# Performance work log

Hardware: AMD Instinct MI355X
Metric: run time of the kernel (lower is better)

Reference implementation:

```python
import jax, jax.numpy as jnp
import numpy as np

B, S, V, L, H, NH, NL = 4, 256, 64, 10, 128, 8, 3
DH = H // NH
LP1 = L + 1


def setup_inputs() -> dict:
    key = jax.random.key(0)
    ks = jax.random.split(key, 18)
    sc = 1.0 / np.sqrt(H)
    return {
        "x": jax.random.normal(ks[0], (B, S, V), jnp.float32),
        "adjacency_logits": jax.random.normal(ks[1], (V, V, LP1), jnp.float32) * 0.1,
        "var_emb": jax.random.normal(ks[2], (V, H), jnp.float32),
        "temp_emb": jax.random.normal(ks[3], (LP1, H), jnp.float32),
        "mech_W": jax.random.normal(ks[4], (V, NL, H, H), jnp.float32) * sc,
        "mech_b": jax.random.normal(ks[5], (V, NL, H), jnp.float32) * 0.01,
        "ln_g": jnp.ones((V, NL, H), jnp.float32),
        "ln_b": jnp.zeros((V, NL, H), jnp.float32),
        "Wq": jax.random.normal(ks[6], (V, H, H), jnp.float32) * sc,
        "Wk": jax.random.normal(ks[7], (V, H, H), jnp.float32) * sc,
        "Wv": jax.random.normal(ks[8], (V, H, H), jnp.float32) * sc,
        "Wo": jax.random.normal(ks[9], (V, H, H), jnp.float32) * sc,
        "bq": jnp.zeros((V, H), jnp.float32),
        "bk": jnp.zeros((V, H), jnp.float32),
        "bv": jnp.zeros((V, H), jnp.float32),
        "bo": jnp.zeros((V, H), jnp.float32),
        "out_W": jax.random.normal(ks[10], (V, H), jnp.float32) * sc,
        "out_b": jnp.zeros((V,), jnp.float32),
    }


def reference(x, adjacency_logits, var_emb, temp_emb, mech_W, mech_b, ln_g, ln_b,
              Wq, Wk, Wv, Wo, bq, bk, bv, bo, out_W, out_b):
    b, s, v = x.shape
    lp1 = adjacency_logits.shape[-1]
    adj = jax.nn.sigmoid(adjacency_logits)  # (V_src, V_tgt, L+1), soft adjacency

    # xlag[b,t,src,l] = x[b, t-l, src] with zero padding (the shift-pad loop, fused)
    xlag = jnp.stack([jnp.pad(x, ((0, 0), (l, 0), (0, 0)))[:, :s] for l in range(lp1)], axis=-1)

    # causal_input[b,t,tgt,h] = sum_{src,l} xlag * adj[src,tgt,l] * (var_emb[src,h] + temp_emb[l,h])
    A = jnp.einsum('btsl,sil->btis', xlag, adj)   # contracted over lag
    Bl = jnp.einsum('btsl,sil->btil', xlag, adj)  # contracted over source
    z = jnp.einsum('btis,sh->btih', A, var_emb) + jnp.einsum('btil,lh->btih', Bl, temp_emb)  # (B,S,V,H)

    # per-variable causal mechanism: Linear -> LayerNorm -> GELU (dropout = identity at eval)
    eps = 1e-5
    nl = mech_W.shape[1]
    for li in range(nl):
        z = jnp.einsum('btvh,vhk->btvk', z, mech_W[:, li]) + mech_b[:, li]
        mu = z.mean(axis=-1, keepdims=True)
        var = z.var(axis=-1, keepdims=True)
        z = (z - mu) / jnp.sqrt(var + eps) * ln_g[:, li] + ln_b[:, li]
        z = jax.nn.gelu(z, approximate=False)

    # per-variable multi-head self-attention over the sequence axis
    def heads(t):
        return t.reshape(b, s, v, NH, DH)
    q = heads(jnp.einsum('btvh,vhk->btvk', z, Wq) + bq)
    k = heads(jnp.einsum('btvh,vhk->btvk', z, Wk) + bk)
    vv = heads(jnp.einsum('btvh,vhk->btvk', z, Wv) + bv)
    scores = jnp.einsum('bqvnd,bkvnd->bvnqk', q, k) / np.sqrt(DH)  # (B,V,NH,S,S)
    attn = jax.nn.softmax(scores, axis=-1)
    o = jnp.einsum('bvnqk,bkvnd->bqvnd', attn, vv).reshape(b, s, v, NH * DH)
    o = jnp.einsum('btvh,vhk->btvk', o, Wo) + bo

    # per-variable output head Linear(H, 1), concatenated over variables
    predictions = jnp.einsum('btvh,vh->btv', o, out_W) + out_b  # (B,S,V)
    return predictions
```

## Files before the change

### kernel.cpp

```cpp
#include <hip/hip_runtime.h>
#include <math.h>

#define BB   4
#define SS   256
#define VV   64
#define LP1  11
#define HH   128
#define NHH  8
#define DHH  16
#define NLL  3
#define BSZ  1024

typedef unsigned short u16;
typedef unsigned int   u32;
typedef __attribute__((ext_vector_type(8))) short s16x8;
typedef __attribute__((ext_vector_type(4))) float f32x4;

__device__ __forceinline__ float bfbits2f(u32 hi16) {
    u32 i = hi16 << 16; float f; __builtin_memcpy(&f, &i, 4); return f;
}
__device__ __forceinline__ u16 f2bf(float f) {
    u32 i; __builtin_memcpy(&i, &f, 4);
    return (u16)((i + 0x7fffu + ((i >> 16) & 1u)) >> 16);
}
__device__ __forceinline__ u16 f2bf_trunc(float f) {
    u32 i; __builtin_memcpy(&i, &f, 4);
    return (u16)(i >> 16);
}
__device__ __forceinline__ u32 cvtpk(float lo, float hi) {
    u32 r;
    asm("v_cvt_pk_bf16_f32 %0, %1, %2" : "=v"(r) : "v"(lo), "v"(hi));
    return r;
}
__device__ __forceinline__ float ldf(const void* p, size_t i, int isbf) {
    if (isbf) return bfbits2f(((const u16*)p)[i]);
    return ((const float*)p)[i];
}
__device__ __forceinline__ float4 ld4(const void* p, size_t i, int isbf) {
    float4 v;
    if (isbf) {
        uint2 u = *(const uint2*)((const u16*)p + i);
        v.x = bfbits2f(u.x & 0xffffu); v.y = bfbits2f(u.x >> 16);
        v.z = bfbits2f(u.y & 0xffffu); v.w = bfbits2f(u.y >> 16);
    } else {
        v = *(const float4*)((const float*)p + i);
    }
    return v;
}
__device__ __forceinline__ void gll16(const u16* g, u16* l) {
    __builtin_amdgcn_global_load_lds(
        (const __attribute__((address_space(1))) void*)g,
        (__attribute__((address_space(3))) void*)l, 16, 0, 0);
}

__global__ __launch_bounds__(64) void k_sniff(const u16* __restrict__ probe,
                                              int* __restrict__ flags) {
    if (threadIdx.x == 0) {
        int wild = 0;
        for (int j = 0; j < 256; j++) {
            float v = bfbits2f(probe[j]);
            if (!(fabsf(v) < 1e8f)) wild = 1;
        }
        flags[0] = wild ? 0 : 1;
    }
}

__global__ __launch_bounds__(256) void k_adj(const void* __restrict__ logits,
                                             float* __restrict__ adj,
                                             const int* __restrict__ flags) {
    int isbf = flags[0];
    int i = blockIdx.x * 256 + threadIdx.x;
    if (i < VV * VV * LP1) {
        float v = ldf(logits, i, isbf);
        adj[i] = 1.f / (1.f + expf(-v));
    }
}

__global__ __launch_bounds__(128) void k_fuse(const void* __restrict__ Wo,
                                              const void* __restrict__ outW,
                                              const void* __restrict__ bo,
                                              const void* __restrict__ outb,
                                              float* __restrict__ wfused,
                                              float* __restrict__ bfused,
                                              const int* __restrict__ flags) {
    int isbf = flags[0];
    int v = blockIdx.x; int h = threadIdx.x;
    __shared__ float ow[HH];
    __shared__ float red[HH];
    ow[h] = ldf(outW, (size_t)v * HH + h, isbf);
    __syncthreads();
    size_t wb = ((size_t)v * HH + h) * HH;
    float acc = 0.f;
    #pragma unroll 8
    for (int k = 0; k < HH; k++) acc += ldf(Wo, wb + k, isbf) * ow[k];
    wfused[v * HH + h] = acc;
    red[h] = ldf(bo, (size_t)v * HH + h, isbf) * ow[h];
    __syncthreads();
    for (int s = 64; s > 0; s >>= 1) { if (h < s) red[h] += red[h + s]; __syncthreads(); }
    if (h == 0) bfused[v] = red[0] + ldf(outb, v, isbf);
}

struct WPack {
    const void* src[6];
    u16* dh[6];
    u16* dl[6];
};
#define TP 136
__global__ __launch_bounds__(256) void k_wprep(WPack wp,
                                               const int* __restrict__ flags) {
    int isbf = flags[0];
    int mat = blockIdx.x;
    int tid = threadIdx.x;
    if (mat >= 384) {
        if (mat == 384) {
            const void* raw = wp.src[4];
            u16* dh = wp.dh[4]; u16* dl = wp.dl[4];
            int n = tid >> 1, half = tid & 1;
            for (int i = 0; i < 32; i++) {
                int s = half * 32 + i;
                float val = ldf(raw, (size_t)s * HH + n, isbf);
                u16 hi = f2bf(val);
                int dst = n * 64 + (s ^ ((n & 7) * 8));
                dh[dst] = hi;
                dl[dst] = f2bf(val - bfbits2f(hi));
            }
        } else {
            const void* raw = wp.src[5];
            u16* dh = wp.dh[5]; u16* dl = wp.dl[5];
            for (int p = tid; p < 8192; p += 256) { dh[p] = 0; dl[p] = 0; }
            __syncthreads();
            if (tid < HH) {
                int n = tid;
                for (int l = 0; l < LP1; l++) {
                    float val = ldf(raw, (size_t)l * HH + n, isbf);
                    u16 hi = f2bf(val);
                    int dst = n * 64 + (l ^ ((n & 7) * 8));
                    dh[dst] = hi;
                    dl[dst] = f2bf(val - bfbits2f(hi));
                }
            }
        }
        return;
    }
    int seg = (mat < 192) ? 0 : 1 + ((mat - 192) >> 6);
    int rel = (mat < 192) ? mat : ((mat - 192) & 63);
    const void* raw = wp.src[seg];
    u16* Wh = wp.dh[seg];
    u16* Wl = wp.dl[seg];
    size_t src = (size_t)rel * (HH * HH);
    if (isbf) {
        __shared__ u16 tile[HH * TP];
        const uint4* sp = (const uint4*)((const u16*)raw + src);
        #pragma unroll
        for (int u = 0; u < 8; u++) {
            int p = u * 256 + tid;
            int h = p >> 4, k8 = (p & 15) * 8;
            int k8s = k8 ^ ((((u32)h >> 3) & 15) * 8);
            *(uint4*)&tile[h * TP + k8s] = sp[p];
        }
        __syncthreads();
        #pragma unroll
        for (int u = 0; u < 8; u++) {
            int p = u * 256 + tid;
            int kcol = p >> 4, h8 = (p & 15) * 8;
            u16 vals[8];
            #pragma unroll
            for (int j = 0; j < 8; j++) {
                int h = h8 + j;
                int ks = kcol ^ ((((u32)h >> 3) & 15) * 8);
                vals[j] = tile[h * TP + ks];
            }
            uint4 pk;
            pk.x = (u32)vals[0] | ((u32)vals[1] << 16);
            pk.y = (u32)vals[2] | ((u32)vals[3] << 16);
            pk.z = (u32)vals[4] | ((u32)vals[5] << 16);
            pk.w = (u32)vals[6] | ((u32)vals[7] << 16);
            int c = h8 >> 6;
            int kloc = (h8 & 63) ^ ((kcol & 7) * 8);
            *(uint4*)&Wh[src + c * 8192 + kcol * 64 + kloc] = pk;
        }
    } else {
        int kcol = tid >> 1, h0 = (tid & 1) * 64;
        for (int i = 0; i < 64; i++) {
            int h = h0 + i;
            float w = ldf(raw, src + (size_t)h * HH + kcol, 0);
            u16 hi = f2bf(w);
            int c = h >> 6;
            size_t dst = src + c * 8192 + (size_t)kcol * 64 + ((h & 63) ^ ((kcol & 7) * 8));
            Wh[dst] = hi;
            Wl[dst] = f2bf(w - bfbits2f(hi));
        }
    }
}

#define PB  72
__global__ __launch_bounds__(256) void k_mega(
    const void* __restrict__ x, const float* __restrict__ adjp,
    const u16* __restrict__ VeH, const u16* __restrict__ VeL,
    const u16* __restrict__ TeH, const u16* __restrict__ TeL,
    const u16* __restrict__ WmH, const u16* __restrict__ WmL,
    const u16* __restrict__ WqH, const u16* __restrict__ WqL,
    const u16* __restrict__ WkH, const u16* __restrict__ WkL,
    const u16* __restrict__ WvH, const u16* __restrict__ WvL,
    const void* __restrict__ mechb,
    const void* __restrict__ lng, const void* __restrict__ lnb,
    const void* __restrict__ bq, const void* __restrict__ bk,
    const void* __restrict__ bv,
    u16* __restrict__ Qh, u16* __restrict__ Ql,
    u16* __restrict__ Ko, u16* __restrict__ Vt,
    const int* __restrict__ flags)
{
    __shared__ __align__(16) u16 SMEM[32768];
    u16* Az_h = SMEM;
    u16* Az_l = SMEM + 8192;
    u16* BdS  = SMEM + 16384;
    u16* Vt_sh = BdS;

    int isbf = flags[0];
    int wexact = isbf;
    int tid = threadIdx.x;
    int bid = blockIdx.x;
    int xcd = bid & 7, idx = bid >> 3;
    int v = xcd * 8 + (idx >> 4);
    int tile = idx & 15;
    int b = tile >> 2, t0 = (tile & 3) * 64;
    int wave = tid >> 6, lane = tid & 63;
    int quad = lane >> 4, l15 = lane & 15;
    int m0 = wave * 16;
    int swzl = (l15 & 7) * 8;

    float* xt = (float*)SMEM;
    for (int p = tid; p < 74 * 64; p += 256) {
        int rr = p >> 6, s = p & 63;
        int trow = t0 - 10 + rr;
        float val = (trow >= 0) ? ldf(x, (size_t)(b * SS + trow) * VV + s, isbf) : 0.f;
        xt[s * 81 + rr] = val;
    }
    __syncthreads();

    float* A_f = (float*)BdS;
    float* Blp = A_f + 64 * 68;
    float* Blf = Blp + 64 * 44;
    {
        int t = lane;
        int sg = wave;
        float blp[LP1];
        #pragma unroll
        for (int l = 0; l < LP1; l++) blp[l] = 0.f;
        for (int k = 0; k < 16; k++) {
            int s = sg * 16 + k;
            const float* ap = adjp + (s * VV + v) * LP1;
            float xw[LP1];
            #pragma unroll
            for (int j = 0; j < LP1; j++) xw[j] = xt[s * 81 + t + j];
            float a = 0.f;
            #pragma unroll
            for (int l = 0; l < LP1; l++) {
                float pr = xw[10 - l] * ap[l];
                a += pr; blp[l] += pr;
            }
            A_f[t * 68 + s] = a;
        }
        #pragma unroll
        for (int l = 0; l < LP1; l++) Blp[t * 44 + sg * 11 + l] = blp[l];
    }
    __syncthreads();
    {
        int t = tid >> 2, c0 = (tid & 3) * 4;
        #pragma unroll
        for (int c = c0; c < c0 + 4; c++) {
            float s4 = 0.f;
            if (c < LP1)
                s4 = (Blp[t * 44 + c] + Blp[t * 44 + 11 + c]) +
                     (Blp[t * 44 + 22 + c] + Blp[t * 44 + 33 + c]);
            Blf[t * 16 + c] = s4;
        }
    }
    __syncthreads();

    s16x8 ahf[2], alf[2], blh, bll;
    #pragma unroll
    for (int kk = 0; kk < 2; kk++) {
        #pragma unroll
        for (int j = 0; j < 8; j++) {
            float a = A_f[(m0 + l15) * 68 + kk * 32 + quad * 8 + j];
            u32 w = cvtpk(a, a);
            u16 hi = (u16)(w & 0xffffu);
            ahf[kk][j] = (short)hi;
            float res = a - bfbits2f(hi);
            alf[kk][j] = (short)(cvtpk(res, res) & 0xffffu);
        }
    }
    #pragma unroll
    for (int j = 0; j < 8; j++) {
        float a = (quad < 2) ? Blf[(m0 + l15) * 16 + quad * 8 + j] : 0.f;
        u32 w = cvtpk(a, a);
        u16 hi = (u16)(w & 0xffffu);
        blh[j] = (short)hi;
        float res = a - bfbits2f(hi);
        bll[j] = (short)(cvtpk(res, res) & 0xffffu);
    }
    __syncthreads();

    auto stageB = [&](u16* dst, const u16* g) {
        const u16* gl = g + wave * 2048 + lane * 8;
        u16* lb = dst + wave * 2048;
        #pragma unroll
        for (int u = 0; u < 4; u++)
            gll16(gl + u * 512, lb + u * 512);
    };

    f32x4 acc[8];
    #pragma unroll
    for (int nt = 0; nt < 8; nt++) {
        f32x4 zz = {0.f, 0.f, 0.f, 0.f};
        acc[nt] = zz;
    }

    if (wexact) {
        stageB(BdS, VeH);
        stageB(BdS + 8192, TeH);
        __syncthreads();
        #pragma unroll
        for (int kk = 0; kk < 2; kk++) {
            int bcol = (kk * 32 + quad * 8) ^ swzl;
            #pragma unroll
            for (int nt = 0; nt < 8; nt++) {
                s16x8 bh = *(const s16x8*)&BdS[(nt * 16 + l15) * 64 + bcol];
                acc[nt] = __builtin_amdgcn_mfma_f32_16x16x32_bf16(ahf[kk], bh, acc[nt], 0, 0, 0);
                acc[nt] = __builtin_amdgcn_mfma_f32_16x16x32_bf16(alf[kk], bh, acc[nt], 0, 0, 0);
            }
        }
        {
            int bcol = (quad * 8) ^ swzl;
            #pragma unroll
            for (int nt = 0; nt < 8; nt++) {
                s16x8 th = *(const s16x8*)&BdS[8192 + (nt * 16 + l15) * 64 + bcol];
                acc[nt] = __builtin_amdgcn_mfma_f32_16x16x32_bf16(blh, th, acc[nt], 0, 0, 0);
                acc[nt] = __builtin_amdgcn_mfma_f32_16x16x32_bf16(bll, th, acc[nt], 0, 0, 0);
            }
        }
    } else {
        stageB(BdS, VeH);
        stageB(BdS + 8192, VeL);
        __syncthreads();
        #pragma unroll
        for (int kk = 0; kk < 2; kk++) {
            int bcol = (kk * 32 + quad * 8) ^ swzl;
            #pragma unroll
            for (int nt = 0; nt < 8; nt++) {
                s16x8 bh = *(const s16x8*)&BdS[(nt * 16 + l15) * 64 + bcol];
                s16x8 bl = *(const s16x8*)&BdS[8192 + (nt * 16 + l15) * 64 + bcol];
                acc[nt] = __builtin_amdgcn_mfma_f32_16x16x32_bf16(ahf[kk], bh, acc[nt], 0, 0, 0);
                acc[nt] = __builtin_amdgcn_mfma_f32_16x16x32_bf16(alf[kk], bh, acc[nt], 0, 0, 0);
                acc[nt] = __builtin_amdgcn_mfma_f32_16x16x32_bf16(ahf[kk], bl, acc[nt], 0, 0, 0);
            }
        }
        __syncthreads();
        stageB(BdS, TeH);
        stageB(BdS + 8192, TeL);
        __syncthreads();
        {
            int bcol = (quad * 8) ^ swzl;
            #pragma unroll
            for (int nt = 0; nt < 8; nt++) {
                s16x8 th = *(const s16x8*)&BdS[(nt * 16 + l15) * 64 + bcol];
                s16x8 tl = *(const s16x8*)&BdS[8192 + (nt * 16 + l15) * 64 + bcol];
                acc[nt] = __builtin_amdgcn_mfma_f32_16x16x32_bf16(blh, th, acc[nt], 0, 0, 0);
                acc[nt] = __builtin_amdgcn_mfma_f32_16x16x32_bf16(bll, th, acc[nt], 0, 0, 0);
                acc[nt] = __builtin_amdgcn_mfma_f32_16x16x32_bf16(blh, tl, acc[nt], 0, 0, 0);
            }
        }
    }
    __syncthreads();

    #pragma unroll
    for (int r = 0; r < 4; r++) {
        int rloc = m0 + quad * 4 + r;
        int swr = (rloc & 7) * 8;
        #pragma unroll
        for (int nt = 0; nt < 8; nt++) {
            float val = acc[nt][r];
            float sx = __shfl_xor(val, 1);
            u32 w = cvtpk(val, sx);
            float res = val - bfbits2f(w & 0xffffu);
            float rx = __shfl_xor(res, 1);
            u32 wl = cvtpk(res, rx);
            if (!(l15 & 1)) {
                int colw = (nt * 16 + (l15 & ~1)) ^ swr;
                *(u32*)&Az_h[rloc * 128 + colw] = w;
                *(u32*)&Az_l[rloc * 128 + colw] = wl;
            }
        }
    }

    int shift = wexact ? 1 : 2;
    int PER = 1 << shift;
    int NCH = 6 << shift;

    auto wchunk = [&](int ch) -> const u16* {
        int li = ch >> shift;
        int sub = ch & (PER - 1);
        int cc = sub & 1, lo = sub >> 1;
        const u16* p; size_t wb;
        if (li < 3)       { p = lo ? WmL : WmH; wb = (size_t)(v * NLL + li) * 16384; }
        else if (li == 3) { p = lo ? WqL : WqH; wb = (size_t)v * 16384; }
        else if (li == 4) { p = lo ? WkL : WkH; wb = (size_t)v * 16384; }
        else              { p = lo ? WvL : WvH; wb = (size_t)v * 16384; }
        return p + wb + cc * 8192;
    };

    auto epilogue = [&](int li) {
        float bcol[8], gcol[8], b2col[8];
        #pragma unroll
        for (int nt = 0; nt < 8; nt++) {
            int col = nt * 16 + l15;
            if (li < 3) {
                size_t pb = (size_t)v * (NLL * HH) + (size_t)li * HH + col;
                bcol[nt]  = ldf(mechb, pb, isbf);
                gcol[nt]  = ldf(lng, pb, isbf);
                b2col[nt] = ldf(lnb, pb, isbf);
            } else {
                const void* bp = (li == 3) ? bq : (li == 4) ? bk : bv;
                bcol[nt] = ldf(bp, (size_t)v * HH + col, isbf);
            }
        }
        if (li == 5) __syncthreads();
        #pragma unroll
        for (int r = 0; r < 4; r++) {
            float vals[8];
            float sum = 0.f, sq = 0.f;
            #pragma unroll
            for (int nt = 0; nt < 8; nt++) {
                float val = acc[nt][r] + bcol[nt];
                vals[nt] = val; sum += val; sq += val * val;
            }
            int rloc = m0 + quad * 4 + r;
            if (li < 3) {
                #pragma unroll
                for (int m = 1; m < 16; m <<= 1) {
                    sum += __shfl_xor(sum, m);
                    sq  += __shfl_xor(sq, m);
                }
                float mean = sum * (1.f / HH);
                float var  = sq * (1.f / HH) - mean * mean;
                float rstd = rsqrtf(var + 1e-5f);
                int swr = (rloc & 7) * 8;
                #pragma unroll
                for (int nt = 0; nt < 8; nt++) {
                    float y = (vals[nt] - mean) * rstd * gcol[nt] + b2col[nt];
                    y = 0.5f * y * (1.f + erff(y * 0.70710678118654752f));
                    float sx = __shfl_xor(y, 1);
                    u32 w = cvtpk(y, sx);
                    float res = y - bfbits2f(w & 0xffffu);
                    float rx = __shfl_xor(res, 1);
                    u32 wl = cvtpk(res, rx);
                    if (!(l15 & 1)) {
                        int colw = (nt * 16 + (l15 & ~1)) ^ swr;
                        *(u32*)&Az_h[rloc * 128 + colw] = w;
                        *(u32*)&Az_l[rloc * 128 + colw] = wl;
                    }
                }
            } else if (li == 3) {
                int row = tile * 64 + rloc;
                size_t ob = ((size_t)v * BSZ + row) * HH;
                #pragma unroll
                for (int nt = 0; nt < 8; nt++) {
                    float val = vals[nt];
                    float sx = __shfl_xor(val, 1);
                    u32 w = cvtpk(val, sx);
                    float res = val - bfbits2f(w & 0xffffu);
                    float rx = __shfl_xor(res, 1);
                    u32 wl = cvtpk(res, rx);
                    if (!(l15 & 1)) {
                        size_t oi = ob + nt * 16 + (l15 & ~1);
                        *(u32*)&Qh[oi] = w;
                        *(u32*)&Ql[oi] = wl;
                    }
                }
            } else if (li == 4) {
                int row = tile * 64 + rloc;
                size_t ob = ((size_t)v * BSZ + row) * HH;
                #pragma unroll
                for (int nt = 0; nt < 8; nt++) {
                    u32 h = f2bf(vals[nt]);
                    u32 hx = (u32)__shfl_xor((int)h, 1);
                    if (!(l15 & 1))
                        *(u32*)&Ko[ob + nt * 16 + (l15 & ~1)] = h | (hx << 16);
                }
            } else {
                #pragma unroll
                for (int nt = 0; nt < 8; nt++)
                    Vt_sh[(nt * 16 + l15) * PB + rloc] = f2bf(vals[nt]);
            }
        }
        if (li == 5) {
            __syncthreads();
            int col = tid >> 1, half = tid & 1;
            int n = col >> 4, d = col & 15;
            int bb = tile >> 2, tq = (tile & 3) * 64;
            size_t dst = (((size_t)(v * BB + bb) * NHH + n) * DHH + d) * SS + tq + half * 32;
            #pragma unroll
            for (int j = 0; j < 4; j++)
                *(uint4*)&Vt[dst + j * 8] = *(const uint4*)&Vt_sh[col * PB + half * 32 + j * 8];
        }
    };

    stageB(BdS, wchunk(0));
    __syncthreads();

    for (int ch = 0; ch < NCH; ch++) {
        int bsel = ch & 1;
        if (ch + 1 < NCH) stageB(BdS + (bsel ^ 1) * 8192, wchunk(ch + 1));
        int sub = ch & (PER - 1);
        int li = ch >> shift;
        int cc = sub & 1, lo = sub >> 1;
        if (sub == 0) {
            #pragma unroll
            for (int nt = 0; nt < 8; nt++) {
                f32x4 zz = {0.f, 0.f, 0.f, 0.f};
                acc[nt] = zz;
            }
        }
        const u16* Bp = BdS + bsel * 8192;
        #pragma unroll
        for (int kk = 0; kk < 2; kk++) {
            int acol = (cc * 64 + kk * 32 + quad * 8) ^ swzl;
            int bcol = (kk * 32 + quad * 8) ^ swzl;
            s16x8 ah = *(const s16x8*)&Az_h[(m0 + l15) * 128 + acol];
            if (!lo) {
                s16x8 al = *(const s16x8*)&Az_l[(m0 + l15) * 128 + acol];
                #pragma unroll
                for (int nt = 0; nt < 8; nt++) {
                    s16x8 bh = *(const s16x8*)&Bp[(nt * 16 + l15) * 64 + bcol];
                    acc[nt] = __builtin_amdgcn_mfma_f32_16x16x32_bf16(ah, bh, acc[nt], 0, 0, 0);
                    acc[nt] = __builtin_amdgcn_mfma_f32_16x16x32_bf16(al, bh, acc[nt], 0, 0, 0);
                }
            } else {
                #pragma unroll
                for (int nt = 0; nt < 8; nt++) {
                    s16x8 bl = *(const s16x8*)&Bp[(nt * 16 + l15) * 64 + bcol];
                    acc[nt] = __builtin_amdgcn_mfma_f32_16x16x32_bf16(ah, bl, acc[nt], 0, 0, 0);
                }
            }
        }
        if (sub == PER - 1) epilogue(li);
        __syncthreads();
    }
}

#define LDW 40
__global__ __launch_bounds__(256) void k_attn2(const u16* __restrict__ Qh,
                                               const u16* __restrict__ Ql,
                                               const u16* __restrict__ K16,
                                               const u16* __restrict__ Vt,
                                               float* __restrict__ O) {
    __shared__ u16 Kp_sh[SS * LDW];
    __shared__ u16 Vt_sh[DHH * 264];
    __shared__ u16 P_sh[4][16 * LDW];
    int tid = threadIdx.x;
    int wave = tid >> 6, lane = tid & 63;
    int quad = lane >> 4, l15 = lane & 15;
    int bn = blockIdx.x, v = blockIdx.y;
    int b = bn >> 3, n = bn & 7;
    size_t qkbase = ((size_t)v * BSZ + b * SS) * HH + n * DHH;
    size_t vtbase = ((size_t)(v * BB + b) * NHH + n) * DHH * SS;

    {
        int row = tid;
        uint4 k0 = *(const uint4*)&K16[qkbase + (size_t)row * HH];
        uint4 k1 = *(const uint4*)&K16[qkbase + (size_t)row * HH + 8];
        *(uint4*)&Kp_sh[row * LDW + 0]  = k0;
        *(uint4*)&Kp_sh[row * LDW + 8]  = k1;
        *(uint4*)&Kp_sh[row * LDW + 16] = k0;
        *(uint4*)&Kp_sh[row * LDW + 24] = k1;
    }
    #pragma unroll
    for (int u = 0; u < 2; u++) {
        int p = u * 256 + tid;
        int d = p >> 5, su = (p & 31) * 8;
        *(uint4*)&Vt_sh[d * 264 + su] = *(const uint4*)&Vt[vtbase + (size_t)d * SS + su];
    }
    __syncthreads();

    s16x8 ones;
    #pragma unroll
    for (int i = 0; i < 8; i++) ones[i] = (short)0x3F80;

    for (int mt = wave * 4; mt < wave * 4 + 4; mt++) {
        const u16* Qsrc = (quad < 2) ? Qh : Ql;
        s16x8 aq = *(const s16x8*)&Qsrc[qkbase + (size_t)(mt * 16 + l15) * HH + (quad & 1) * 8];
        f32x4 oacc = {0.f, 0.f, 0.f, 0.f};
        f32x4 lacc = {0.f, 0.f, 0.f, 0.f};
        for (int jt2 = 0; jt2 < 8; jt2++) {
            #pragma unroll
            for (int sub = 0; sub < 2; sub++) {
                int jt = jt2 * 2 + sub;
                s16x8 bk = *(const s16x8*)&Kp_sh[(jt * 16 + l15) * LDW + quad * 8];
                f32x4 s = {0.f, 0.f, 0.f, 0.f};
                s = __builtin_amdgcn_mfma_f32_16x16x32_bf16(aq, bk, s, 0, 0, 0);
                #pragma unroll
                for (int r = 0; r < 4; r++) {
                    float p = __expf(s[r] * 0.25f);
                    P_sh[wave][(quad * 4 + r) * LDW + sub * 16 + l15] = f2bf_trunc(p);
                }
            }
            s16x8 ap = *(const s16x8*)&P_sh[wave][l15 * LDW + quad * 8];
            s16x8 bv = *(const s16x8*)&Vt_sh[l15 * 264 + jt2 * 32 + quad * 8];
            oacc = __builtin_amdgcn_mfma_f32_16x16x32_bf16(ap, bv, oacc, 0, 0, 0);
            lacc = __builtin_amdgcn_mfma_f32_16x16x32_bf16(ap, ones, lacc, 0, 0, 0);
        }
        #pragma unroll
        for (int r = 0; r < 4; r++) {
            float val = oacc[r] / lacc[r];
            O[((size_t)v * BSZ + b * SS + mt * 16 + quad * 4 + r) * HH + n * DHH + l15] = val;
        }
    }
}

__global__ __launch_bounds__(256) void k_final(const float* __restrict__ o,
                                               const float* __restrict__ wfused,
                                               const float* __restrict__ bfused,
                                               void* __restrict__ out,
                                               const int* __restrict__ flags) {
    __shared__ float wf[HH];
    int isbf = flags[0];
    int tid = threadIdx.x; int b = blockIdx.x; int v = blockIdx.y;
    if (tid < HH) wf[tid] = wfused[v * HH + tid];
    __syncthreads();
    int rg = tid >> 3;
    int l8 = tid & 7;
    float4 w0 = *(const float4*)&wf[l8 * 16];
    float4 w1 = *(const float4*)&wf[l8 * 16 + 4];
    float4 w2 = *(const float4*)&wf[l8 * 16 + 8];
    float4 w3 = *(const float4*)&wf[l8 * 16 + 12];
    float bv = bfused[v];
    #pragma unroll
    for (int pass = 0; pass < 8; pass++) {
        int bt = b * SS + pass * 32 + rg;
        const float4* orow = (const float4*)(o + ((size_t)v * BSZ + bt) * HH + l8 * 16);
        float4 a0 = orow[0], a1 = orow[1], a2 = orow[2], a3 = orow[3];
        float acc = a0.x * w0.x + a0.y * w0.y + a0.z * w0.z + a0.w * w0.w
                  + a1.x * w1.x + a1.y * w1.y + a1.z * w1.z + a1.w * w1.w
                  + a2.x * w2.x + a2.y * w2.y + a2.z * w2.z + a2.w * w2.w
                  + a3.x * w3.x + a3.y * w3.y + a3.z * w3.z + a3.w * w3.w;
        acc += __shfl_xor(acc, 1);
        acc += __shfl_xor(acc, 2);
        acc += __shfl_xor(acc, 4);
        if (l8 == 0) {
            float pred = acc + bv;
            size_t oi = (size_t)bt * VV + v;
            if (isbf) ((u16*)out)[oi] = f2bf(pred);
            else      ((float*)out)[oi] = pred;
        }
    }
}

extern "C" void kernel_launch(void* const* d_in, const int* in_sizes, int n_in,
                              void* d_out, int out_size, void* d_ws, size_t ws_size,
                              hipStream_t stream) {
    (void)out_size; (void)ws_size;

    static const int dict_sizes[18]  = {65536,45056,8192,1408,3145728,24576,24576,24576,
                                        1048576,1048576,1048576,1048576,8192,8192,8192,8192,8192,64};
    static const int alpha_sizes[18] = {1048576,1048576,1048576,1048576,45056,8192,8192,8192,
                                        8192,24576,24576,3145728,24576,8192,64,1408,8192,65536};
    static const int alpha_pos[18]   = {17,4,16,15,11,12,10,9,2,0,3,1,7,5,8,6,13,14};
    static const int alpha_logical[18] = {9,11,8,10,1,13,15,12,14,7,6,4,5,16,17,3,2,0};

    const void* in[18];
    bool is_dict = (n_in == 18), is_alpha = (n_in == 18);
    for (int i = 0; i < 18 && i < n_in; i++) {
        if (in_sizes[i] != dict_sizes[i])  is_dict = false;
        if (in_sizes[i] != alpha_sizes[i]) is_alpha = false;
    }
    if (is_dict) {
        for (int i = 0; i < 18; i++) in[i] = d_in[i];
    } else if (is_alpha) {
        for (int i = 0; i < 18; i++) in[i] = d_in[alpha_pos[i]];
    } else {
        bool used[18] = {false};
        for (int a = 0; a < 18; a++) {
            int lg = alpha_logical[a];
            for (int i = 0; i < n_in && i < 18; i++) {
                if (!used[i] && in_sizes[i] == dict_sizes[lg]) {
                    in[lg] = d_in[i]; used[i] = true; break;
                }
            }
        }
    }

    const void* x        = in[0];
    const void* adjl     = in[1];
    const void* var_emb  = in[2];
    const void* temp_emb = in[3];
    const void* mechW    = in[4];
    const void* mechb    = in[5];
    const void* lng      = in[6];
    const void* lnb      = in[7];
    const void* Wq       = in[8];
    const void* Wk       = in[9];
    const void* Wv       = in[10];
    const void* Wo       = in[11];
    const void* bq       = in[12];
    const void* bk       = in[13];
    const void* bv       = in[14];
    const void* bo       = in[15];
    const void* outW     = in[16];
    const void* outb     = in[17];

    float* ws     = (float*)d_ws;
    int*   flags  = (int*)ws;
    float* adj    = ws + 32;
    float* wfused = ws + 45088;
    float* bfused = ws + 53280;
    float* Obuf   = ws + 53376;
    u16*   zhB    = (u16*)(ws + 8441984);
    u16*   zlB    = (u16*)(ws + 12636288);
    u16*   K16    = (u16*)(ws + 16830592);
    u16*   Vt16   = (u16*)(ws + 21024896);
    u16*   WtmH   = (u16*)(ws + 25219200);
    u16*   WtmL   = (u16*)(ws + 26792064);
    u16*   WtqH   = (u16*)(ws + 28364928);
    u16*   WtqL   = (u16*)(ws + 28889216);
    u16*   WtkH   = (u16*)(ws + 29413504);
    u16*   WtkL   = (u16*)(ws + 29937792);
    u16*   WtvH   = (u16*)(ws + 30462080);
    u16*   WtvL   = (u16*)(ws + 30986368);
    u16*   WveH   = (u16*)(ws + 31510656);
    u16*   WveL   = (u16*)(ws + 31514752);
    u16*   WteH   = (u16*)(ws + 31518848);
    u16*   WteL   = (u16*)(ws + 31522944);

    k_sniff <<<dim3(1),    dim3(64),  0, stream>>>((const u16*)mechW, flags);
    k_adj   <<<dim3(176),  dim3(256), 0, stream>>>(adjl, adj, flags);
    k_fuse  <<<dim3(64),   dim3(128), 0, stream>>>(Wo, outW, bo, outb, wfused, bfused, flags);

    WPack wp;
    wp.src[0] = mechW;    wp.dh[0] = WtmH; wp.dl[0] = WtmL;
    wp.src[1] = Wq;       wp.dh[1] = WtqH; wp.dl[1] = WtqL;
    wp.src[2] = Wk;       wp.dh[2] = WtkH; wp.dl[2] = WtkL;
    wp.src[3] = Wv;       wp.dh[3] = WtvH; wp.dl[3] = WtvL;
    wp.src[4] = var_emb;  wp.dh[4] = WveH; wp.dl[4] = WveL;
    wp.src[5] = temp_emb; wp.dh[5] = WteH; wp.dl[5] = WteL;
    k_wprep <<<dim3(386),  dim3(256), 0, stream>>>(wp, flags);

    k_mega<<<dim3(1024), dim3(256), 0, stream>>>(
            x, adj,
            WveH, WveL, WteH, WteL,
            WtmH, WtmL, WtqH, WtqL, WtkH, WtkL, WtvH, WtvL,
            mechb, lng, lnb, bq, bk, bv,
            zhB, zlB, K16, Vt16, flags);

    k_attn2 <<<dim3(BB * NHH, VV), dim3(256), 0, stream>>>(zhB, zlB, K16, Vt16, Obuf);
    k_final <<<dim3(BB, VV), dim3(256), 0, stream>>>(Obuf, wfused, bfused, d_out, flags);
}
```

Baseline: 403.0 us.

## Triple-buffer weight chunks in mega kernel with fine-grained vmcnt waits

Replaces the double-buffered weight staging with a three-slot LDS ring so weight chunks are prefetched two iterations ahead. Explicit s_waitcnt vmcnt values and raw s_barrier replace __syncthreads, and chunk 0 is prefetched during the embedding GEMM. Per-layer bias and LayerNorm parameter loads are hoisted out of the epilogue to the start of each layer, and s_setprio raises wave priority around the MFMA loops. LDS use grows from 64KB to 80KB per block, which can lower occupancy, and hand-set vmcnt counts depend on the exact number of outstanding loads, so any miscount would cause a data race.

```diff
diff --git a/kernel.cpp b/kernel.cpp
--- a/kernel.cpp
+++ b/kernel.cpp
@@ -210,11 +210,11 @@
     u16* __restrict__ Ko, u16* __restrict__ Vt,
     const int* __restrict__ flags)
 {
-    __shared__ __align__(16) u16 SMEM[32768];
+    __shared__ __align__(16) u16 SMEM[40960];
     u16* Az_h = SMEM;
     u16* Az_l = SMEM + 8192;
-    u16* BdS  = SMEM + 16384;
-    u16* Vt_sh = BdS;
+    u16* ring = SMEM + 16384;
+    u16* Vt_sh = ring;
 
     int isbf = flags[0];
     int wexact = isbf;
@@ -238,7 +238,7 @@
     }
     __syncthreads();
 
-    float* A_f = (float*)BdS;
+    float* A_f = (float*)ring;
     float* Blp = A_f + 64 * 68;
     float* Blf = Blp + 64 * 44;
     {
@@ -310,6 +310,22 @@
             gll16(gl + u * 512, lb + u * 512);
     };
 
+    int shift = wexact ? 1 : 2;
+    int PER = 1 << shift;
+    int NCH = 6 << shift;
+
+    auto wchunk = [&](int ch) -> const u16* {
+        int li = ch >> shift;
+        int sub = ch & (PER - 1);
+        int cc = sub & 1, lo = sub >> 1;
+        const u16* p; size_t wb;
+        if (li < 3)       { p = lo ? WmL : WmH; wb = (size_t)(v * NLL + li) * 16384; }
+        else if (li == 3) { p = lo ? WqL : WqH; wb = (size_t)v * 16384; }
+        else if (li == 4) { p = lo ? WkL : WkH; wb = (size_t)v * 16384; }
+        else              { p = lo ? WvL : WvH; wb = (size_t)v * 16384; }
+        return p + wb + cc * 8192;
+    };
+
     f32x4 acc[8];
     #pragma unroll
     for (int nt = 0; nt < 8; nt++) {
@@ -318,15 +334,18 @@
     }
 
     if (wexact) {
-        stageB(BdS, VeH);
-        stageB(BdS + 8192, TeH);
-        __syncthreads();
+        stageB(ring, VeH);
+        stageB(ring + 8192, TeH);
+        stageB(ring + 16384, wchunk(0));
+        asm volatile("s_waitcnt vmcnt(4) lgkmcnt(0)" ::: "memory");
+        __builtin_amdgcn_s_barrier();
+        __builtin_amdgcn_s_setprio(1);
         #pragma unroll
         for (int kk = 0; kk < 2; kk++) {
             int bcol = (kk * 32 + quad * 8) ^ swzl;
             #pragma unroll
             for (int nt = 0; nt < 8; nt++) {
-                s16x8 bh = *(const s16x8*)&BdS[(nt * 16 + l15) * 64 + bcol];
+                s16x8 bh = *(const s16x8*)&ring[(nt * 16 + l15) * 64 + bcol];
                 acc[nt] = __builtin_amdgcn_mfma_f32_16x16x32_bf16(ahf[kk], bh, acc[nt], 0, 0, 0);
                 acc[nt] = __builtin_amdgcn_mfma_f32_16x16x32_bf16(alf[kk], bh, acc[nt], 0, 0, 0);
             }
@@ -335,44 +354,46 @@
             int bcol = (quad * 8) ^ swzl;
             #pragma unroll
             for (int nt = 0; nt < 8; nt++) {
-                s16x8 th = *(const s16x8*)&BdS[8192 + (nt * 16 + l15) * 64 + bcol];
+                s16x8 th = *(const s16x8*)&ring[8192 + (nt * 16 + l15) * 64 + bcol];
                 acc[nt] = __builtin_amdgcn_mfma_f32_16x16x32_bf16(blh, th, acc[nt], 0, 0, 0);
                 acc[nt] = __builtin_amdgcn_mfma_f32_16x16x32_bf16(bll, th, acc[nt], 0, 0, 0);
             }
         }
+        __builtin_amdgcn_s_setprio(0);
     } else {
-        stageB(BdS, VeH);
-        stageB(BdS + 8192, VeL);
+        stageB(ring, VeH);
+        stageB(ring + 8192, VeL);
         __syncthreads();
         #pragma unroll
         for (int kk = 0; kk < 2; kk++) {
             int bcol = (kk * 32 + quad * 8) ^ swzl;
             #pragma unroll
             for (int nt = 0; nt < 8; nt++) {
-                s16x8 bh = *(const s16x8*)&BdS[(nt * 16 + l15) * 64 + bcol];
-                s16x8 bl = *(const s16x8*)&BdS[8192 + (nt * 16 + l15) * 64 + bcol];
+                s16x8 bh = *(const s16x8*)&ring[(nt * 16 + l15) * 64 + bcol];
+                s16x8 bl = *(const s16x8*)&ring[8192 + (nt * 16 + l15) * 64 + bcol];
                 acc[nt] = __builtin_amdgcn_mfma_f32_16x16x32_bf16(ahf[kk], bh, acc[nt], 0, 0, 0);
                 acc[nt] = __builtin_amdgcn_mfma_f32_16x16x32_bf16(alf[kk], bh, acc[nt], 0, 0, 0);
                 acc[nt] = __builtin_amdgcn_mfma_f32_16x16x32_bf16(ahf[kk], bl, acc[nt], 0, 0, 0);
             }
         }
         __syncthreads();
-        stageB(BdS, TeH);
-        stageB(BdS + 8192, TeL);
+        stageB(ring, TeH);
+        stageB(ring + 8192, TeL);
         __syncthreads();
         {
             int bcol = (quad * 8) ^ swzl;
             #pragma unroll
             for (int nt = 0; nt < 8; nt++) {
-                s16x8 th = *(const s16x8*)&BdS[(nt * 16 + l15) * 64 + bcol];
-                s16x8 tl = *(const s16x8*)&BdS[8192 + (nt * 16 + l15) * 64 + bcol];
+                s16x8 th = *(const s16x8*)&ring[(nt * 16 + l15) * 64 + bcol];
+                s16x8 tl = *(const s16x8*)&ring[8192 + (nt * 16 + l15) * 64 + bcol];
                 acc[nt] = __builtin_amdgcn_mfma_f32_16x16x32_bf16(blh, th, acc[nt], 0, 0, 0);
                 acc[nt] = __builtin_amdgcn_mfma_f32_16x16x32_bf16(bll, th, acc[nt], 0, 0, 0);
                 acc[nt] = __builtin_amdgcn_mfma_f32_16x16x32_bf16(blh, tl, acc[nt], 0, 0, 0);
             }
         }
-    }
-    __syncthreads();
+        __syncthreads();
+        stageB(ring + 16384, wchunk(0));
+    }
 
     #pragma unroll
     for (int r = 0; r < 4; r++) {
@@ -394,37 +415,9 @@
         }
     }
 
-    int shift = wexact ? 1 : 2;
-    int PER = 1 << shift;
-    int NCH = 6 << shift;
-
-    auto wchunk = [&](int ch) -> const u16* {
-        int li = ch >> shift;
-        int sub = ch & (PER - 1);
-        int cc = sub & 1, lo = sub >> 1;
-        const u16* p; size_t wb;
-        if (li < 3)       { p = lo ? WmL : WmH; wb = (size_t)(v * NLL + li) * 16384; }
-        else if (li == 3) { p = lo ? WqL : WqH; wb = (size_t)v * 16384; }
-        else if (li == 4) { p = lo ? WkL : WkH; wb = (size_t)v * 16384; }
-        else              { p = lo ? WvL : WvH; wb = (size_t)v * 16384; }
-        return p + wb + cc * 8192;
-    };
+    float bcol[8], gcol[8], b2col[8];
 
     auto epilogue = [&](int li) {
-        float bcol[8], gcol[8], b2col[8];
-        #pragma unroll
-        for (int nt = 0; nt < 8; nt++) {
-            int col = nt * 16 + l15;
-            if (li < 3) {
-                size_t pb = (size_t)v * (NLL * HH) + (size_t)li * HH + col;
-                bcol[nt]  = ldf(mechb, pb, isbf);
-                gcol[nt]  = ldf(lng, pb, isbf);
-                b2col[nt] = ldf(lnb, pb, isbf);
-            } else {
-                const void* bp = (li == 3) ? bq : (li == 4) ? bk : bv;
-                bcol[nt] = ldf(bp, (size_t)v * HH + col, isbf);
-            }
-        }
         if (li == 5) __syncthreads();
         #pragma unroll
         for (int r = 0; r < 4; r++) {
@@ -506,46 +499,71 @@
         }
     };
 
-    stageB(BdS, wchunk(0));
-    __syncthreads();
-
     for (int ch = 0; ch < NCH; ch++) {
-        int bsel = ch & 1;
-        if (ch + 1 < NCH) stageB(BdS + (bsel ^ 1) * 8192, wchunk(ch + 1));
         int sub = ch & (PER - 1);
         int li = ch >> shift;
         int cc = sub & 1, lo = sub >> 1;
+
+        if (ch == 0 && NCH > 1) stageB(ring + ((1 + 2) % 3) * 8192, wchunk(1));
+        if (ch + 2 < NCH)       stageB(ring + ((ch + 4) % 3) * 8192, wchunk(ch + 2));
+
+        int ahead = NCH - 1 - ch; if (ahead > 2) ahead = 2;
+        if (ahead == 2)      asm volatile("s_waitcnt vmcnt(8) lgkmcnt(0)" ::: "memory");
+        else if (ahead == 1) asm volatile("s_waitcnt vmcnt(4) lgkmcnt(0)" ::: "memory");
+        else                 asm volatile("s_waitcnt vmcnt(0) lgkmcnt(0)" ::: "memory");
+        __builtin_amdgcn_s_barrier();
+        __builtin_amdgcn_sched_barrier(0);
+
         if (sub == 0) {
             #pragma unroll
             for (int nt = 0; nt < 8; nt++) {
                 f32x4 zz = {0.f, 0.f, 0.f, 0.f};
                 acc[nt] = zz;
             }
-        }
-        const u16* Bp = BdS + bsel * 8192;
+            #pragma unroll
+            for (int nt = 0; nt < 8; nt++) {
+                int col = nt * 16 + l15;
+                if (li < 3) {
+                    size_t pb = (size_t)v * (NLL * HH) + (size_t)li * HH + col;
+                    bcol[nt]  = ldf(mechb, pb, isbf);
+                    gcol[nt]  = ldf(lng, pb, isbf);
+                    b2col[nt] = ldf(lnb, pb, isbf);
+                } else {
+                    const void* bp = (li == 3) ? bq : (li == 4) ? bk : bv;
+                    bcol[nt] = ldf(bp, (size_t)v * HH + col, isbf);
+                }
+            }
+        }
+
+        const u16* Bp = ring + ((ch + 2) % 3) * 8192;
+        __builtin_amdgcn_s_setprio(1);
         #pragma unroll
         for (int kk = 0; kk < 2; kk++) {
             int acol = (cc * 64 + kk * 32 + quad * 8) ^ swzl;
-            int bcol = (kk * 32 + quad * 8) ^ swzl;
+            int bcol2 = (kk * 32 + quad * 8) ^ swzl;
             s16x8 ah = *(const s16x8*)&Az_h[(m0 + l15) * 128 + acol];
             if (!lo) {
                 s16x8 al = *(const s16x8*)&Az_l[(m0 + l15) * 128 + acol];
                 #pragma unroll
                 for (int nt = 0; nt < 8; nt++) {
-                    s16x8 bh = *(const s16x8*)&Bp[(nt * 16 + l15) * 64 + bcol];
+                    s16x8 bh = *(const s16x8*)&Bp[(nt * 16 + l15) * 64 + bcol2];
                     acc[nt] = __builtin_amdgcn_mfma_f32_16x16x32_bf16(ah, bh, acc[nt], 0, 0, 0);
                     acc[nt] = __builtin_amdgcn_mfma_f32_16x16x32_bf16(al, bh, acc[nt], 0, 0, 0);
                 }
             } else {
                 #pragma unroll
                 for (int nt = 0; nt < 8; nt++) {
-                    s16x8 bl = *(const s16x8*)&Bp[(nt * 16 + l15) * 64 + bcol];
+                    s16x8 bl = *(const s16x8*)&Bp[(nt * 16 + l15) * 64 + bcol2];
                     acc[nt] = __builtin_amdgcn_mfma_f32_16x16x32_bf16(ah, bl, acc[nt], 0, 0, 0);
                 }
             }
         }
+        __builtin_amdgcn_s_setprio(0);
+
         if (sub == PER - 1) epilogue(li);
-        __syncthreads();
+
+        asm volatile("s_waitcnt lgkmcnt(0)" ::: "memory");
+        __builtin_amdgcn_s_barrier();
     }
 }
 
```

Result: slower. 534.6 us (+32.6%).
